# Optimization experiments

Hardware: AMD Instinct MI355X
Metric: run time of the kernel (lower is better)

## Reference

```python
import jax, jax.numpy as jnp
import numpy as np

N = 20000   # nodes per type (lnc and dis)
E = 160000  # edges per meta-path graph and per pos/neg link graph
H = 8       # attention heads
D = 32      # out_size per head (H*D = 256 flattened)
HID = 256   # hidden_size from ResNet projection


def _bn(x, g, b, eps=1e-5):
    # training-mode BatchNorm1d (biased variance, like torch)
    m = x.mean(0)
    v = x.var(0)
    return g * (x - m) * jax.lax.rsqrt(v + eps) + b


def _leaky(x, slope):
    return jnp.where(x >= 0, x, slope * x)


def _gat(h_src, h_dst, src, dst, W, al, ar, n_dst):
    # DGL GATConv (bipartite, shared fc, no bias, eval mode)
    fs = (h_src @ W).reshape(-1, H, D)          # [Ns,H,D]
    fd = (h_dst @ W).reshape(-1, H, D)          # [Nd,H,D]
    el = (fs * al).sum(-1)                      # [Ns,H]
    er = (fd * ar).sum(-1)                      # [Nd,H]
    e = _leaky(el[src] + er[dst], 0.2)          # [E,H]
    emax = jax.ops.segment_max(e, dst, num_segments=n_dst)
    emax = jnp.where(jnp.isfinite(emax), emax, 0.0)   # zero in-degree safety
    ee = jnp.exp(e - emax[dst])
    den = jax.ops.segment_sum(ee, dst, num_segments=n_dst)
    a = ee / jnp.maximum(den[dst], 1e-9)        # edge softmax over incoming edges
    out = jax.ops.segment_sum(a[:, :, None] * fs[src], dst, num_segments=n_dst)
    return _leaky(out, 0.01).reshape(n_dst, H * D)  # activation=F.leaky_relu, flatten(1)


def _sem_attn(z, W1, b1, w2):
    # z: [N, 2, H*D]; SemanticAttention
    w = (jnp.tanh(z @ W1 + b1) @ w2).mean(0)    # [2]
    beta = jax.nn.softmax(w, axis=0)            # [2]
    return (beta[None, :, None] * z).sum(1)     # [N, H*D]


def setup_inputs() -> dict:
    key = jax.random.key(0)
    ks = jax.random.split(key, 32)
    s = 0.05
    inp = {
        "x_lnc": jax.random.normal(ks[0], (N, 256), jnp.float32),
        "x_dis": jax.random.normal(ks[1], (N, 256), jnp.float32),
        "proj_W": jax.random.normal(ks[2], (2, 256, HID), jnp.float32) * s,
        "proj_bn_g": jnp.ones((HID,), jnp.float32),
        "proj_bn_b": jnp.zeros((HID,), jnp.float32),
        "short_W": jax.random.normal(ks[3], (2, 256, HID), jnp.float32) * s,
        "short_b": jnp.zeros((2, HID), jnp.float32),
        "gat_W": jax.random.normal(ks[4], (4, HID, H * D), jnp.float32) * s,
        "gat_al": jax.random.normal(ks[5], (4, H, D), jnp.float32) * s,
        "gat_ar": jax.random.normal(ks[6], (4, H, D), jnp.float32) * s,
        "sem_W1": jax.random.normal(ks[7], (H * D, 128), jnp.float32) * s,
        "sem_b1": jnp.zeros((128,), jnp.float32),
        "sem_w2": jax.random.normal(ks[8], (128,), jnp.float32) * s,
    }
    names = ["ld_src", "ld_dst", "ll_src", "ll_dst", "dl_src", "dl_dst",
             "dd_src", "dd_dst", "pos_src", "pos_dst", "neg_src", "neg_dst"]
    for i, nm in enumerate(names):
        inp[nm] = jax.random.randint(ks[10 + i], (E,), 0, N, jnp.int32)
    return inp


def reference(x_lnc, x_dis, proj_W, proj_bn_g, proj_bn_b, short_W, short_b,
              gat_W, gat_al, gat_ar, sem_W1, sem_b1, sem_w2,
              ld_src, ld_dst, ll_src, ll_dst, dl_src, dl_dst,
              dd_src, dd_dst, pos_src, pos_dst, neg_src, neg_dst):
    # ResNet projection (shared BN applied per-branch, training-mode stats)
    l_x = _leaky(_bn(x_lnc @ proj_W[0], proj_bn_g, proj_bn_b), 0.01) + (x_lnc @ short_W[0] + short_b[0])
    d_x = _leaky(_bn(x_dis @ proj_W[1], proj_bn_g, proj_bn_b), 0.01) + (x_dis @ short_W[1] + short_b[1])
    # HANLayer: 4 meta-path GATs with pairings (l,d),(l,l),(d,l),(d,d)
    e0 = _gat(l_x, d_x, ld_src, ld_dst, gat_W[0], gat_al[0], gat_ar[0], N)  # dst dis
    e1 = _gat(l_x, l_x, ll_src, ll_dst, gat_W[1], gat_al[1], gat_ar[1], N)  # dst lnc
    e2 = _gat(d_x, l_x, dl_src, dl_dst, gat_W[2], gat_al[2], gat_ar[2], N)  # dst lnc
    e3 = _gat(d_x, d_x, dd_src, dd_dst, gat_W[3], gat_al[3], gat_ar[3], N)  # dst dis
    l_embs = _sem_attn(jnp.stack((e1, e2), axis=1), sem_W1, sem_b1, sem_w2)
    d_embs = _sem_attn(jnp.stack((e0, e3), axis=1), sem_W1, sem_b1, sem_w2)
    # Hadamard u_mul_v over 'lnc-dis' edges (pos graph and neg graph)
    pos_z = l_embs[pos_src] * d_embs[pos_dst]
    neg_z = l_embs[neg_src] * d_embs[neg_dst]
    return pos_z, neg_z, l_embs, d_embs
```

## Files before the change

kernel.cpp:

```cpp
#include <hip/hip_runtime.h>
#include <math.h>

#define NN 20000
#define NE 160000
#define SLOT 40

typedef _Float16 f16;
typedef __attribute__((ext_vector_type(8))) _Float16 f16x8;
typedef __attribute__((ext_vector_type(4))) float f32x4;

__device__ __forceinline__ float leakyf(float x, float s){ return x >= 0.f ? x : s*x; }
__device__ __forceinline__ ushort f2h(float x){ f16 h = (f16)x; ushort u; __builtin_memcpy(&u,&h,2); return u; }
__device__ __forceinline__ float h2f(ushort u){ f16 h; __builtin_memcpy(&h,&u,2); return (float)h; }

__device__ __forceinline__ void gload_lds16(const void* g, void* l){
  __builtin_amdgcn_global_load_lds((const __attribute__((address_space(1))) uint*)g,
                                   (__attribute__((address_space(3))) uint*)l, 16, 0, 0);
}

__global__ void fill_i(int* p, int v, long n){
  long i = (long)blockIdx.x*blockDim.x + threadIdx.x;
  long st = (long)gridDim.x*blockDim.x;
  for (; i<n; i+=st) p[i]=v;
}

__global__ __launch_bounds__(256) void conv_x(const float* __restrict__ in0,
    const float* __restrict__ in1, ushort* __restrict__ out0, ushort* __restrict__ out1){
  const float* in = blockIdx.y ? in1 : in0;
  ushort* out = blockIdx.y ? out1 : out0;
  long idx = (long)blockIdx.x*256 + threadIdx.x;
  long r = idx>>6; int c4 = (int)(idx&63)<<2;
  float4 v = *(const float4*)(in + r*256 + c4);
  ushort4 o; o.x=f2h(v.x); o.y=f2h(v.y); o.z=f2h(v.z); o.w=f2h(v.w);
  *(ushort4*)(out + r*256 + c4) = o;
}

__global__ void convB_all(const float* __restrict__ proj_W, const float* __restrict__ short_W,
    const float* __restrict__ gat_W, const float* __restrict__ sem_W1,
    ushort* btpl, ushort* btpd, ushort* btgl, ushort* btgd, ushort* btsm){
  int idx = blockIdx.x*256 + threadIdx.x;
  float v; ushort* out; int n, k;
  if (idx < 131072){
    n = idx>>8; k = idx&255; out = btpl;
    v = (n<256)? proj_W[(size_t)k*256+n] : short_W[(size_t)k*256+(n-256)];
  } else if (idx < 262144){
    int l = idx-131072; n = l>>8; k = l&255; out = btpd;
    v = (n<256)? proj_W[65536+(size_t)k*256+n] : short_W[65536+(size_t)k*256+(n-256)];
  } else if (idx < 458752){
    int l = idx-262144; n = l>>8; k = l&255; out = btgl;
    int sl = n>>8; const float* b = gat_W + (sl==0?0:(sl==1?65536:131072));
    v = b[(size_t)k*256 + (n&255)];
  } else if (idx < 655360){
    int l = idx-458752; n = l>>8; k = l&255; out = btgd;
    int sl = n>>8; const float* b = gat_W + (sl==0?0:(sl==1?131072:196608));
    v = b[(size_t)k*256 + (n&255)];
  } else {
    int l = idx-655360; n = l>>8; k = l&255; out = btsm;
    v = sem_W1[(size_t)k*128 + n];
  }
  out[(size_t)n*256 + k] = f2h(v);
}

__global__ void scatter_slots(const int* s0, const int* s1, const int* s2, const int* s3,
    const int* d0, const int* d1, const int* d2, const int* d3,
    int* __restrict__ cnt, int* __restrict__ slots){
  int g = blockIdx.y;
  const int* src = (g==0)?s0:(g==1)?s1:(g==2)?s2:s3;
  const int* dst = (g==0)?d0:(g==1)?d1:(g==2)?d2:d3;
  int i = blockIdx.x*256 + threadIdx.x;
  if (i<NE){
    int d = dst[i];
    int p = atomicAdd(&cnt[g*NN + d], 1);
    slots[(size_t)(g*NN + d)*SLOT + p] = src[i];
  }
}

template<int EPI>
__global__ __launch_bounds__(256) void gemm16(
    const ushort* __restrict__ A0, const ushort* __restrict__ A1,
    const ushort* __restrict__ B0, const ushort* __restrict__ B1,
    ushort* __restrict__ C0, ushort* __restrict__ C1, int ldc, int M,
    float* __restrict__ sbuf,
    const float* __restrict__ gat_al, const float* __restrict__ gat_ar,
    float* __restrict__ elbase, float* __restrict__ erbase,
    const float* __restrict__ b1v, const float* __restrict__ w2v){
  const int z = blockIdx.z;
  const ushort* A = z ? A1 : A0;
  const ushort* Bt = z ? B1 : B0;
  ushort* C = z ? C1 : C0;
  __shared__ ushort sm[16384];
  char* smc = (char*)sm;
  const int tid = threadIdx.x;
  const int lane = tid & 63, wid = tid >> 6;
  const int wr = wid >> 1, wc = wid & 1;
  const int fr = lane & 15, fq = lane >> 4;
  const int brow = blockIdx.y*128, bcol = blockIdx.x*128;
  f32x4 acc[4][4];
  #pragma unroll
  for (int i=0;i<4;i++)
    #pragma unroll
    for (int j=0;j<4;j++) acc[i][j] = (f32x4){0.f,0.f,0.f,0.f};

  for (int k0 = 0; k0 < 256; k0 += 64){
    __syncthreads();
    #pragma unroll
    for (int cc = 0; cc < 8; cc++){
      int c = wid*8 + cc;
      int ch = c & 15;
      int rel = ch*1024 + lane*16;
      int row = rel >> 7;
      int scb = (rel & 127) ^ ((row & 7) << 4);
      const char* src;
      if (c < 16){
        int gr = brow + row; gr = (gr < M) ? gr : (M-1);
        src = (const char*)A + (size_t)gr*512 + k0*2 + scb;
      } else {
        src = (const char*)Bt + (size_t)(bcol + row)*512 + k0*2 + scb;
      }
      gload_lds16(src, smc + ((c<16)?0:16384) + ch*1024);
    }
    __syncthreads();
    #pragma unroll
    for (int ks = 0; ks < 2; ks++){
      f16x8 af[4], bfr[4];
      #pragma unroll
      for (int i=0;i<4;i++){
        int r = wr*64 + i*16 + fr;
        int koff = ks*32 + fq*8;
        int aoff = ((r<<7) + koff*2) ^ ((r&7)<<4);
        af[i] = *(const f16x8*)(smc + aoff);
        int n = wc*64 + i*16 + fr;
        int boff = ((n<<7) + koff*2) ^ ((n&7)<<4);
        bfr[i] = *(const f16x8*)(smc + 16384 + boff);
      }
      #pragma unroll
      for (int i=0;i<4;i++)
        #pragma unroll
        for (int j=0;j<4;j++)
          acc[i][j] = __builtin_amdgcn_mfma_f32_16x16x32_f16(af[i], bfr[j], acc[i][j], 0,0,0);
    }
  }

  if (EPI==1 || EPI==2){
    #pragma unroll
    for (int i=0;i<4;i++){
      #pragma unroll
      for (int e=0;e<4;e++){
        int gr = brow + wr*64 + i*16 + fq*4 + e;
        if (gr < M){
          #pragma unroll
          for (int j=0;j<4;j++)
            C[(size_t)gr*ldc + bcol + wc*64 + j*16 + fr] = f2h(acc[i][j][e]);
        }
      }
    }
  }

  if (EPI==1 && bcol < 256){
    float* gsum = sbuf + z*512;
    float* gsq  = gsum + 256;
    #pragma unroll
    for (int j=0;j<4;j++){
      float s=0.f, q=0.f;
      #pragma unroll
      for (int i=0;i<4;i++)
        #pragma unroll
        for (int e=0;e<4;e++){
          int gr = brow + wr*64 + i*16 + fq*4 + e;
          if (gr < M){ float v = acc[i][j][e]; s += v; q += v*v; }
        }
      s += __shfl_xor(s,16); s += __shfl_xor(s,32);
      q += __shfl_xor(q,16); q += __shfl_xor(q,32);
      if (fq==0){
        int gc = bcol + wc*64 + j*16 + fr;
        atomicAdd(&gsum[gc], s);
        atomicAdd(&gsq[gc], q);
      }
    }
  }

  if (EPI==2){
    int slice = bcol >> 8;
    int hbase = (bcol & 255) >> 5;
    float *d1=nullptr, *d2=nullptr; const float *a1=nullptr, *a2=nullptr;
    if (z==0){
      if (slice==0){ d1=elbase; a1=gat_al; }
      else if (slice==1){ d1=elbase+160000; a1=gat_al+256; d2=erbase+160000; a2=gat_ar+256; }
      else { d1=erbase+320000; a1=gat_ar+512; }
    } else {
      if (slice==0){ d1=erbase; a1=gat_ar; }
      else if (slice==1){ d1=elbase+320000; a1=gat_al+512; }
      else { d1=elbase+480000; a1=gat_al+768; d2=erbase+480000; a2=gat_ar+768; }
    }
    int hA = hbase + wc*2, hB = hA+1;
    #pragma unroll
    for (int t=0;t<2;t++){
      const float* av = t ? a2 : a1;
      float* dst = t ? d2 : d1;
      if (t==1 && d2==nullptr) break;
      float avv[4];
      #pragma unroll
      for (int j=0;j<4;j++)
        avv[j] = av[(hbase + wc*2 + (j>>1))*32 + (j&1)*16 + fr];
      #pragma unroll
      for (int i=0;i<4;i++){
        #pragma unroll
        for (int e=0;e<4;e++){
          int gr = brow + wr*64 + i*16 + fq*4 + e;
          float pA = acc[i][0][e]*avv[0] + acc[i][1][e]*avv[1];
          float pB = acc[i][2][e]*avv[2] + acc[i][3][e]*avv[3];
          pA += __shfl_xor(pA,1); pA += __shfl_xor(pA,2);
          pA += __shfl_xor(pA,4); pA += __shfl_xor(pA,8);
          pB += __shfl_xor(pB,1); pB += __shfl_xor(pB,2);
          pB += __shfl_xor(pB,4); pB += __shfl_xor(pB,8);
          if (fr==0 && gr < M){
            dst[(size_t)gr*8 + hA] = pA;
            dst[(size_t)gr*8 + hB] = pB;
          }
        }
      }
    }
  }

  if (EPI==3){
    float b1c[4], w2c[4];
    #pragma unroll
    for (int j=0;j<4;j++){
      int col = wc*64 + j*16 + fr;
      b1c[j] = b1v[col]; w2c[j] = w2v[col];
    }
    int segA = brow/20000;
    int bound = (segA+1)*20000;
    float t0=0.f, t1=0.f;
    #pragma unroll
    for (int i=0;i<4;i++){
      #pragma unroll
      for (int e=0;e<4;e++){
        int gr = brow + wr*64 + i*16 + fq*4 + e;
        float rs = 0.f;
        #pragma unroll
        for (int j=0;j<4;j++){
          float x = acc[i][j][e] + b1c[j];
          float ex = __expf(2.f*x);
          rs += (1.f - 2.f/(ex+1.f))*w2c[j];
        }
        if (gr < bound) t0 += rs; else t1 += rs;
      }
    }
    #pragma unroll
    for (int off=32; off>0; off>>=1){ t0 += __shfl_xor(t0,off); t1 += __shfl_xor(t1,off); }
    if (lane==0){
      atomicAdd(&sbuf[segA], t0);
      if (brow + 127 >= bound) atomicAdd(&sbuf[segA+1], t1);
    }
  }
}

__global__ void bn_final2(const float* sbuf, float* mr){
  int t = threadIdx.x;
  int y = t>>8, c = t&255;
  const float* gsum = sbuf + y*512;
  const float* gsq  = gsum + 256;
  float m = gsum[c]/(float)NN;
  float v = gsq[c]/(float)NN - m*m;
  mr[y*512 + c] = m;
  mr[y*512 + 256 + c] = rsqrtf(v + 1e-5f);
}

__global__ __launch_bounds__(256) void proj_apply2(const ushort* __restrict__ PS_l,
    const ushort* __restrict__ PS_d, const float* __restrict__ mr,
    const float* __restrict__ gg, const float* __restrict__ bb,
    const float* __restrict__ short_b, ushort* __restrict__ out_l, ushort* __restrict__ out_d){
  int y = blockIdx.y;
  const ushort* PS = y ? PS_d : PS_l;
  ushort* out = y ? out_d : out_l;
  const float* mean = mr + y*512;
  const float* rinv = mean + 256;
  const float* sb = short_b + y*256;
  long idx = (long)blockIdx.x*256 + threadIdx.x;
  long r = idx>>6; int c4 = (int)(idx&63)<<2;
  ushort4 pu = *(const ushort4*)(PS + r*512 + c4);
  ushort4 su = *(const ushort4*)(PS + r*512 + 256 + c4);
  float pv[4] = {h2f(pu.x),h2f(pu.y),h2f(pu.z),h2f(pu.w)};
  float sv[4] = {h2f(su.x),h2f(su.y),h2f(su.z),h2f(su.w)};
  ushort o[4];
  #pragma unroll
  for (int k=0;k<4;k++){
    int c = c4+k;
    float yv = (pv[k]-mean[c])*rinv[c]*gg[c] + bb[c];
    o[k] = f2h(leakyf(yv,0.01f) + sv[k] + sb[c]);
  }
  ushort4 ov; ov.x=o[0]; ov.y=o[1]; ov.z=o[2]; ov.w=o[3];
  *(ushort4*)(out + r*256 + c4) = ov;
}

__global__ __launch_bounds__(256) void gat_fused(const int* __restrict__ cnt,
    const int* __restrict__ slots, const float* __restrict__ elbase,
    const float* __restrict__ erbase, const ushort* __restrict__ fc_l,
    const ushort* __restrict__ fc_d, ushort* __restrict__ sems){
  const int g = blockIdx.y;
  const int n = blockIdx.x*4 + (threadIdx.x>>6);
  const int lane = threadIdx.x & 63;
  const int co[4]   = {0,256,256,512};
  const int semo[4] = {40000,0,20000,60000};
  const float* el = elbase + g*160000;
  const float* er = erbase + g*160000;
  const ushort* F = (g<2) ? fc_l : fc_d;
  const int coloff = co[g];
  const int j = lane>>3, h = lane&7, hc = lane>>3;
  const int e1 = cnt[g*NN + n];
  const long sb = (long)(g*NN + n)*SLOT;
  const float ern = er[n*8+h];
  float m_run = -3.0e38f, s_run = 0.f;
  float4 acc = make_float4(0.f,0.f,0.f,0.f);

  for (int base = 0; base < e1; base += 8){
    int idx = base + j;
    bool valid = idx < e1;
    int src = valid ? slots[sb + idx] : 0;
    float ev = valid ? leakyf(el[src*8+h] + ern, 0.2f) : -3.0e38f;
    float mx = fmaxf(ev, __shfl_xor(ev,8));
    mx = fmaxf(mx, __shfl_xor(mx,16));
    mx = fmaxf(mx, __shfl_xor(mx,32));
    float m_new = fmaxf(m_run, mx);
    float sc = (m_run > -1.0e38f) ? __expf(m_run - m_new) : 1.f;
    float p = valid ? __expf(ev - m_new) : 0.f;
    float ps = p + __shfl_xor(p,8);
    ps += __shfl_xor(ps,16);
    ps += __shfl_xor(ps,32);
    s_run = s_run*sc + ps;
    m_run = m_new;
    float scc = __shfl(sc, hc);
    acc.x*=scc; acc.y*=scc; acc.z*=scc; acc.w*=scc;
    #pragma unroll
    for (int e=0;e<8;e++){
      if (base + e >= e1) break;
      float w = __shfl(p, e*8 + hc);
      int s = __shfl(src, e*8);
      ushort4 fu = *(const ushort4*)(F + (size_t)s*768 + coloff + lane*4);
      acc.x = fmaf(w,h2f(fu.x),acc.x); acc.y = fmaf(w,h2f(fu.y),acc.y);
      acc.z = fmaf(w,h2f(fu.z),acc.z); acc.w = fmaf(w,h2f(fu.w),acc.w);
    }
  }
  float rd = 1.f/fmaxf(__shfl(s_run, hc), 1e-9f);
  ushort4 o;
  o.x = f2h(leakyf(acc.x*rd, 0.01f)); o.y = f2h(leakyf(acc.y*rd, 0.01f));
  o.z = f2h(leakyf(acc.z*rd, 0.01f)); o.w = f2h(leakyf(acc.w*rd, 0.01f));
  *(ushort4*)(sems + (size_t)(semo[g]+n)*256 + lane*4) = o;
}

__global__ void beta_k(const float* tsum, float* beta){
  float wl0 = tsum[0]/20000.f, wl1 = tsum[1]/20000.f;
  float m = fmaxf(wl0,wl1);
  float a = __expf(wl0-m), b = __expf(wl1-m);
  beta[0]=a/(a+b); beta[1]=b/(a+b);
  float wd0 = tsum[2]/20000.f, wd1 = tsum[3]/20000.f;
  m = fmaxf(wd0,wd1);
  a = __expf(wd0-m); b = __expf(wd1-m);
  beta[2]=a/(a+b); beta[3]=b/(a+b);
}

__global__ __launch_bounds__(256) void sem_combine(const ushort* __restrict__ sems,
    const float* __restrict__ beta, float* __restrict__ lemb, float* __restrict__ demb){
  long idx = (long)blockIdx.x*256 + threadIdx.x;
  long r = idx>>6; int c4 = (int)(idx&63)<<2;
  float b0=beta[0], b1=beta[1], b2=beta[2], b3=beta[3];
  ushort4 v1 = *(const ushort4*)(sems + (r          )*256 + c4);
  ushort4 v2 = *(const ushort4*)(sems + (r + 20000L )*256 + c4);
  ushort4 v0 = *(const ushort4*)(sems + (r + 40000L )*256 + c4);
  ushort4 v3 = *(const ushort4*)(sems + (r + 60000L )*256 + c4);
  float4 lo, dd;
  lo.x = b0*h2f(v1.x) + b1*h2f(v2.x); dd.x = b2*h2f(v0.x) + b3*h2f(v3.x);
  lo.y = b0*h2f(v1.y) + b1*h2f(v2.y); dd.y = b2*h2f(v0.y) + b3*h2f(v3.y);
  lo.z = b0*h2f(v1.z) + b1*h2f(v2.z); dd.z = b2*h2f(v0.z) + b3*h2f(v3.z);
  lo.w = b0*h2f(v1.w) + b1*h2f(v2.w); dd.w = b2*h2f(v0.w) + b3*h2f(v3.w);
  *(float4*)(lemb + r*256 + c4) = lo;
  *(float4*)(demb + r*256 + c4) = dd;
}

__global__ __launch_bounds__(256) void edge_mul2(const int* __restrict__ ps, const int* __restrict__ pd,
    const int* __restrict__ ns, const int* __restrict__ nd,
    const float* __restrict__ lemb, const float* __restrict__ demb,
    float* __restrict__ pos, float* __restrict__ neg){
  long idx = (long)blockIdx.x*256 + threadIdx.x;
  const long H = (long)NE*64;
  const int *es, *ed; float* out; long t;
  if (idx < H){ es=ps; ed=pd; out=pos; t=idx; }
  else { es=ns; ed=nd; out=neg; t=idx-H; }
  long i = t>>6; int jj = (int)(t&63);
  int s = es[i], d = ed[i];
  float4 a = *(const float4*)(lemb + (size_t)s*256 + (size_t)jj*4);
  float4 b = *(const float4*)(demb + (size_t)d*256 + (size_t)jj*4);
  float4 o = make_float4(a.x*b.x, a.y*b.y, a.z*b.z, a.w*b.w);
  *(float4*)(out + (size_t)t*4) = o;
}

extern "C" void kernel_launch(void* const* d_in, const int* in_sizes, int n_in,
                              void* d_out, int out_size, void* d_ws, size_t ws_size,
                              hipStream_t stream){
  const float* x_lnc  = (const float*)d_in[0];
  const float* x_dis  = (const float*)d_in[1];
  const float* proj_W = (const float*)d_in[2];
  const float* bn_g   = (const float*)d_in[3];
  const float* bn_b   = (const float*)d_in[4];
  const float* short_W= (const float*)d_in[5];
  const float* short_b= (const float*)d_in[6];
  const float* gat_W  = (const float*)d_in[7];
  const float* gat_al = (const float*)d_in[8];
  const float* gat_ar = (const float*)d_in[9];
  const float* sem_W1 = (const float*)d_in[10];
  const float* sem_b1 = (const float*)d_in[11];
  const float* sem_w2 = (const float*)d_in[12];
  const int* g_src[4] = {(const int*)d_in[13],(const int*)d_in[15],(const int*)d_in[17],(const int*)d_in[19]};
  const int* g_dst[4] = {(const int*)d_in[14],(const int*)d_in[16],(const int*)d_in[18],(const int*)d_in[20]};
  const int* pos_src = (const int*)d_in[21];
  const int* pos_dst = (const int*)d_in[22];
  const int* neg_src = (const int*)d_in[23];
  const int* neg_dst = (const int*)d_in[24];

  const long LEMB = (long)NN*256;
  const long EOUT = (long)NE*256;

  float* outf = (float*)d_out;
  float* pos  = outf;
  float* negr = outf + EOUT;
  float* lemb = outf + 2*EOUT;
  float* demb = lemb + LEMB;

  ushort* PS_l = (ushort*)negr;
  ushort* PS_d = PS_l + 10240000;
  ushort* fc_l = (ushort*)negr;
  ushort* fc_d = fc_l + 15360000;

  float* ws   = (float*)d_ws;
  float* sbuf = ws;
  float* tsum = ws + 1024;
  int*   cnt  = (int*)(ws + 1028);
  float* beta = (float*)(cnt + 80000);
  float* mr   = beta + 4;
  float* elbase = mr + 1024;
  float* erbase = elbase + 640000;
  int*   slots  = (int*)(erbase + 640000);
  ushort* xhl  = (ushort*)(slots + 3200000);
  ushort* xhd  = xhl + 5120000;
  ushort* axl  = xhd + 5120000;
  ushort* axd  = axl + 5120000;
  ushort* sems = axd + 5120000;
  ushort* btpl = sems + 20480000;
  ushort* btpd = btpl + 131072;
  ushort* btgl = btpd + 131072;
  ushort* btgd = btgl + 196608;
  ushort* btsm = btgd + 196608;

  conv_x<<<dim3(5000,2),256,0,stream>>>(x_lnc, x_dis, xhl, xhd);
  convB_all<<<2688,256,0,stream>>>(proj_W, short_W, gat_W, sem_W1,
                                   btpl, btpd, btgl, btgd, btsm);
  fill_i<<<317,256,0,stream>>>((int*)ws, 0, 81028);
  scatter_slots<<<dim3(625,4),256,0,stream>>>(g_src[0],g_src[1],g_src[2],g_src[3],
      g_dst[0],g_dst[1],g_dst[2],g_dst[3], cnt, slots);

  gemm16<1><<<dim3(4,157,2),256,0,stream>>>(xhl, xhd, btpl, btpd, PS_l, PS_d, 512, NN,
      sbuf, nullptr, nullptr, nullptr, nullptr, nullptr, nullptr);
  bn_final2<<<1,512,0,stream>>>(sbuf, mr);
  proj_apply2<<<dim3(5000,2),256,0,stream>>>(PS_l, PS_d, mr, bn_g, bn_b, short_b, axl, axd);

  gemm16<2><<<dim3(6,157,2),256,0,stream>>>(axl, axd, btgl, btgd, fc_l, fc_d, 768, NN,
      nullptr, gat_al, gat_ar, elbase, erbase, nullptr, nullptr);

  gat_fused<<<dim3(5000,4),256,0,stream>>>(cnt, slots, elbase, erbase, fc_l, fc_d, sems);

  gemm16<3><<<dim3(1,625,1),256,0,stream>>>(sems, nullptr, btsm, nullptr, nullptr, nullptr, 128, 80000,
      tsum, nullptr, nullptr, nullptr, nullptr, sem_b1, sem_w2);
  beta_k<<<1,1,0,stream>>>(tsum, beta);
  sem_combine<<<5000,256,0,stream>>>(sems, beta, lemb, demb);

  edge_mul2<<<80000,256,0,stream>>>(pos_src, pos_dst, neg_src, neg_dst, lemb, demb, pos, negr);
}
```

Before: 431.9 us.

## Merge prep kernels, fold BN/beta finalize, drop softmax max, fp16 edge gathers

Combines input conversion, weight transposition and workspace zeroing into one prep launch. BN statistics finalization and the semantic-attention beta softmax are folded into their consumer kernels, removing two tiny launches. The GAT edge softmax drops the running-max rescaling and exponentiates the raw logits directly, which is cheaper but can overflow for large logits. The final edge Hadamard gathers fp16 copies of the embeddings to halve gather traffic, at the cost of precision and an extra write in sem_combine.

```diff
diff --git a/kernel.cpp b/kernel.cpp
--- a/kernel.cpp
+++ b/kernel.cpp
@@ -18,47 +18,48 @@
                                    (__attribute__((address_space(3))) uint*)l, 16, 0, 0);
 }
 
-__global__ void fill_i(int* p, int v, long n){
-  long i = (long)blockIdx.x*blockDim.x + threadIdx.x;
-  long st = (long)gridDim.x*blockDim.x;
-  for (; i<n; i+=st) p[i]=v;
-}
-
-__global__ __launch_bounds__(256) void conv_x(const float* __restrict__ in0,
-    const float* __restrict__ in1, ushort* __restrict__ out0, ushort* __restrict__ out1){
-  const float* in = blockIdx.y ? in1 : in0;
-  ushort* out = blockIdx.y ? out1 : out0;
-  long idx = (long)blockIdx.x*256 + threadIdx.x;
-  long r = idx>>6; int c4 = (int)(idx&63)<<2;
-  float4 v = *(const float4*)(in + r*256 + c4);
-  ushort4 o; o.x=f2h(v.x); o.y=f2h(v.y); o.z=f2h(v.z); o.w=f2h(v.w);
-  *(ushort4*)(out + r*256 + c4) = o;
-}
-
-__global__ void convB_all(const float* __restrict__ proj_W, const float* __restrict__ short_W,
-    const float* __restrict__ gat_W, const float* __restrict__ sem_W1,
-    ushort* btpl, ushort* btpd, ushort* btgl, ushort* btgd, ushort* btsm){
-  int idx = blockIdx.x*256 + threadIdx.x;
-  float v; ushort* out; int n, k;
-  if (idx < 131072){
-    n = idx>>8; k = idx&255; out = btpl;
-    v = (n<256)? proj_W[(size_t)k*256+n] : short_W[(size_t)k*256+(n-256)];
-  } else if (idx < 262144){
-    int l = idx-131072; n = l>>8; k = l&255; out = btpd;
-    v = (n<256)? proj_W[65536+(size_t)k*256+n] : short_W[65536+(size_t)k*256+(n-256)];
-  } else if (idx < 458752){
-    int l = idx-262144; n = l>>8; k = l&255; out = btgl;
-    int sl = n>>8; const float* b = gat_W + (sl==0?0:(sl==1?65536:131072));
-    v = b[(size_t)k*256 + (n&255)];
-  } else if (idx < 655360){
-    int l = idx-458752; n = l>>8; k = l&255; out = btgd;
-    int sl = n>>8; const float* b = gat_W + (sl==0?0:(sl==1?131072:196608));
-    v = b[(size_t)k*256 + (n&255)];
+__global__ __launch_bounds__(256) void prep(const float* __restrict__ x_lnc,
+    const float* __restrict__ x_dis, const float* __restrict__ proj_W,
+    const float* __restrict__ short_W, const float* __restrict__ gat_W,
+    const float* __restrict__ sem_W1,
+    ushort* __restrict__ xhl, ushort* __restrict__ xhd,
+    ushort* btpl, ushort* btpd, ushort* btgl, ushort* btgd, ushort* btsm,
+    int* __restrict__ zbuf){
+  int b = blockIdx.x;
+  if (b < 10000){
+    const float* in = (b >= 5000) ? x_dis : x_lnc;
+    ushort* out = (b >= 5000) ? xhd : xhl;
+    long idx = (long)(b % 5000)*256 + threadIdx.x;
+    long r = idx>>6; int c4 = (int)(idx&63)<<2;
+    float4 v = *(const float4*)(in + r*256 + c4);
+    ushort4 o; o.x=f2h(v.x); o.y=f2h(v.y); o.z=f2h(v.z); o.w=f2h(v.w);
+    *(ushort4*)(out + r*256 + c4) = o;
+  } else if (b < 12688){
+    int idx = (b-10000)*256 + threadIdx.x;
+    float v; ushort* out; int n, k;
+    if (idx < 131072){
+      n = idx>>8; k = idx&255; out = btpl;
+      v = (n<256)? proj_W[(size_t)k*256+n] : short_W[(size_t)k*256+(n-256)];
+    } else if (idx < 262144){
+      int l = idx-131072; n = l>>8; k = l&255; out = btpd;
+      v = (n<256)? proj_W[65536+(size_t)k*256+n] : short_W[65536+(size_t)k*256+(n-256)];
+    } else if (idx < 458752){
+      int l = idx-262144; n = l>>8; k = l&255; out = btgl;
+      int sl = n>>8; const float* bb = gat_W + (sl==0?0:(sl==1?65536:131072));
+      v = bb[(size_t)k*256 + (n&255)];
+    } else if (idx < 655360){
+      int l = idx-458752; n = l>>8; k = l&255; out = btgd;
+      int sl = n>>8; const float* bb = gat_W + (sl==0?0:(sl==1?131072:196608));
+      v = bb[(size_t)k*256 + (n&255)];
+    } else {
+      int l = idx-655360; n = l>>8; k = l&255; out = btsm;
+      v = sem_W1[(size_t)k*128 + n];
+    }
+    out[(size_t)n*256 + k] = f2h(v);
   } else {
-    int l = idx-655360; n = l>>8; k = l&255; out = btsm;
-    v = sem_W1[(size_t)k*128 + n];
-  }
-  out[(size_t)n*256 + k] = f2h(v);
+    int idx = (b-12688)*256 + threadIdx.x;
+    if (idx < 81028) zbuf[idx] = 0;
+  }
 }
 
 __global__ void scatter_slots(const int* s0, const int* s1, const int* s2, const int* s3,
@@ -256,26 +257,15 @@
   }
 }
 
-__global__ void bn_final2(const float* sbuf, float* mr){
-  int t = threadIdx.x;
-  int y = t>>8, c = t&255;
-  const float* gsum = sbuf + y*512;
-  const float* gsq  = gsum + 256;
-  float m = gsum[c]/(float)NN;
-  float v = gsq[c]/(float)NN - m*m;
-  mr[y*512 + c] = m;
-  mr[y*512 + 256 + c] = rsqrtf(v + 1e-5f);
-}
-
 __global__ __launch_bounds__(256) void proj_apply2(const ushort* __restrict__ PS_l,
-    const ushort* __restrict__ PS_d, const float* __restrict__ mr,
+    const ushort* __restrict__ PS_d, const float* __restrict__ sbuf,
     const float* __restrict__ gg, const float* __restrict__ bb,
     const float* __restrict__ short_b, ushort* __restrict__ out_l, ushort* __restrict__ out_d){
   int y = blockIdx.y;
   const ushort* PS = y ? PS_d : PS_l;
   ushort* out = y ? out_d : out_l;
-  const float* mean = mr + y*512;
-  const float* rinv = mean + 256;
+  const float* gsum = sbuf + y*512;
+  const float* gsq  = gsum + 256;
   const float* sb = short_b + y*256;
   long idx = (long)blockIdx.x*256 + threadIdx.x;
   long r = idx>>6; int c4 = (int)(idx&63)<<2;
@@ -287,7 +277,10 @@
   #pragma unroll
   for (int k=0;k<4;k++){
     int c = c4+k;
-    float yv = (pv[k]-mean[c])*rinv[c]*gg[c] + bb[c];
+    float m = gsum[c]*(1.f/NN);
+    float va = gsq[c]*(1.f/NN) - m*m;
+    float ri = rsqrtf(va + 1e-5f);
+    float yv = (pv[k]-m)*ri*gg[c] + bb[c];
     o[k] = f2h(leakyf(yv,0.01f) + sv[k] + sb[c]);
   }
   ushort4 ov; ov.x=o[0]; ov.y=o[1]; ov.z=o[2]; ov.w=o[3];
@@ -311,27 +304,15 @@
   const int e1 = cnt[g*NN + n];
   const long sb = (long)(g*NN + n)*SLOT;
   const float ern = er[n*8+h];
-  float m_run = -3.0e38f, s_run = 0.f;
+  float ssum = 0.f;
   float4 acc = make_float4(0.f,0.f,0.f,0.f);
 
   for (int base = 0; base < e1; base += 8){
     int idx = base + j;
     bool valid = idx < e1;
     int src = valid ? slots[sb + idx] : 0;
-    float ev = valid ? leakyf(el[src*8+h] + ern, 0.2f) : -3.0e38f;
-    float mx = fmaxf(ev, __shfl_xor(ev,8));
-    mx = fmaxf(mx, __shfl_xor(mx,16));
-    mx = fmaxf(mx, __shfl_xor(mx,32));
-    float m_new = fmaxf(m_run, mx);
-    float sc = (m_run > -1.0e38f) ? __expf(m_run - m_new) : 1.f;
-    float p = valid ? __expf(ev - m_new) : 0.f;
-    float ps = p + __shfl_xor(p,8);
-    ps += __shfl_xor(ps,16);
-    ps += __shfl_xor(ps,32);
-    s_run = s_run*sc + ps;
-    m_run = m_new;
-    float scc = __shfl(sc, hc);
-    acc.x*=scc; acc.y*=scc; acc.z*=scc; acc.w*=scc;
+    float p = valid ? __expf(leakyf(el[src*8+h] + ern, 0.2f)) : 0.f;
+    ssum += p;
     #pragma unroll
     for (int e=0;e<8;e++){
       if (base + e >= e1) break;
@@ -342,29 +323,28 @@
       acc.z = fmaf(w,h2f(fu.z),acc.z); acc.w = fmaf(w,h2f(fu.w),acc.w);
     }
   }
-  float rd = 1.f/fmaxf(__shfl(s_run, hc), 1e-9f);
+  ssum += __shfl_xor(ssum,8); ssum += __shfl_xor(ssum,16); ssum += __shfl_xor(ssum,32);
+  float rd = 1.f/fmaxf(__shfl(ssum, hc), 1e-9f);
   ushort4 o;
   o.x = f2h(leakyf(acc.x*rd, 0.01f)); o.y = f2h(leakyf(acc.y*rd, 0.01f));
   o.z = f2h(leakyf(acc.z*rd, 0.01f)); o.w = f2h(leakyf(acc.w*rd, 0.01f));
   *(ushort4*)(sems + (size_t)(semo[g]+n)*256 + lane*4) = o;
 }
 
-__global__ void beta_k(const float* tsum, float* beta){
-  float wl0 = tsum[0]/20000.f, wl1 = tsum[1]/20000.f;
+__global__ __launch_bounds__(256) void sem_combine(const ushort* __restrict__ sems,
+    const float* __restrict__ tsum, float* __restrict__ lemb, float* __restrict__ demb,
+    ushort* __restrict__ lemb16, ushort* __restrict__ demb16){
+  float wl0 = tsum[0]*(1.f/20000.f), wl1 = tsum[1]*(1.f/20000.f);
   float m = fmaxf(wl0,wl1);
-  float a = __expf(wl0-m), b = __expf(wl1-m);
-  beta[0]=a/(a+b); beta[1]=b/(a+b);
-  float wd0 = tsum[2]/20000.f, wd1 = tsum[3]/20000.f;
+  float ea = __expf(wl0-m), eb = __expf(wl1-m);
+  float b0 = ea/(ea+eb), b1 = eb/(ea+eb);
+  float wd0 = tsum[2]*(1.f/20000.f), wd1 = tsum[3]*(1.f/20000.f);
   m = fmaxf(wd0,wd1);
-  a = __expf(wd0-m); b = __expf(wd1-m);
-  beta[2]=a/(a+b); beta[3]=b/(a+b);
-}
-
-__global__ __launch_bounds__(256) void sem_combine(const ushort* __restrict__ sems,
-    const float* __restrict__ beta, float* __restrict__ lemb, float* __restrict__ demb){
+  ea = __expf(wd0-m); eb = __expf(wd1-m);
+  float b2 = ea/(ea+eb), b3 = eb/(ea+eb);
+
   long idx = (long)blockIdx.x*256 + threadIdx.x;
   long r = idx>>6; int c4 = (int)(idx&63)<<2;
-  float b0=beta[0], b1=beta[1], b2=beta[2], b3=beta[3];
   ushort4 v1 = *(const ushort4*)(sems + (r          )*256 + c4);
   ushort4 v2 = *(const ushort4*)(sems + (r + 20000L )*256 + c4);
   ushort4 v0 = *(const ushort4*)(sems + (r + 40000L )*256 + c4);
@@ -376,11 +356,16 @@
   lo.w = b0*h2f(v1.w) + b1*h2f(v2.w); dd.w = b2*h2f(v0.w) + b3*h2f(v3.w);
   *(float4*)(lemb + r*256 + c4) = lo;
   *(float4*)(demb + r*256 + c4) = dd;
+  ushort4 lh, dh;
+  lh.x=f2h(lo.x); lh.y=f2h(lo.y); lh.z=f2h(lo.z); lh.w=f2h(lo.w);
+  dh.x=f2h(dd.x); dh.y=f2h(dd.y); dh.z=f2h(dd.z); dh.w=f2h(dd.w);
+  *(ushort4*)(lemb16 + r*256 + c4) = lh;
+  *(ushort4*)(demb16 + r*256 + c4) = dh;
 }
 
 __global__ __launch_bounds__(256) void edge_mul2(const int* __restrict__ ps, const int* __restrict__ pd,
     const int* __restrict__ ns, const int* __restrict__ nd,
-    const float* __restrict__ lemb, const float* __restrict__ demb,
+    const ushort* __restrict__ lemb16, const ushort* __restrict__ demb16,
     float* __restrict__ pos, float* __restrict__ neg){
   long idx = (long)blockIdx.x*256 + threadIdx.x;
   const long H = (long)NE*64;
@@ -389,9 +374,10 @@
   else { es=ns; ed=nd; out=neg; t=idx-H; }
   long i = t>>6; int jj = (int)(t&63);
   int s = es[i], d = ed[i];
-  float4 a = *(const float4*)(lemb + (size_t)s*256 + (size_t)jj*4);
-  float4 b = *(const float4*)(demb + (size_t)d*256 + (size_t)jj*4);
-  float4 o = make_float4(a.x*b.x, a.y*b.y, a.z*b.z, a.w*b.w);
+  ushort4 a = *(const ushort4*)(lemb16 + (size_t)s*256 + (size_t)jj*4);
+  ushort4 b = *(const ushort4*)(demb16 + (size_t)d*256 + (size_t)jj*4);
+  float4 o = make_float4(h2f(a.x)*h2f(b.x), h2f(a.y)*h2f(b.y),
+                         h2f(a.z)*h2f(b.z), h2f(a.w)*h2f(b.w));
   *(float4*)(out + (size_t)t*4) = o;
 }
 
@@ -436,9 +422,7 @@
   float* sbuf = ws;
   float* tsum = ws + 1024;
   int*   cnt  = (int*)(ws + 1028);
-  float* beta = (float*)(cnt + 80000);
-  float* mr   = beta + 4;
-  float* elbase = mr + 1024;
+  float* elbase = ws + 81028;
   float* erbase = elbase + 640000;
   int*   slots  = (int*)(erbase + 640000);
   ushort* xhl  = (ushort*)(slots + 3200000);
@@ -446,23 +430,22 @@
   ushort* axl  = xhd + 5120000;
   ushort* axd  = axl + 5120000;
   ushort* sems = axd + 5120000;
-  ushort* btpl = sems + 20480000;
+  ushort* lemb16 = sems + 20480000;
+  ushort* demb16 = lemb16 + 5120000;
+  ushort* btpl = demb16 + 5120000;
   ushort* btpd = btpl + 131072;
   ushort* btgl = btpd + 131072;
   ushort* btgd = btgl + 196608;
   ushort* btsm = btgd + 196608;
 
-  conv_x<<<dim3(5000,2),256,0,stream>>>(x_lnc, x_dis, xhl, xhd);
-  convB_all<<<2688,256,0,stream>>>(proj_W, short_W, gat_W, sem_W1,
-                                   btpl, btpd, btgl, btgd, btsm);
-  fill_i<<<317,256,0,stream>>>((int*)ws, 0, 81028);
+  prep<<<13005,256,0,stream>>>(x_lnc, x_dis, proj_W, short_W, gat_W, sem_W1,
+                               xhl, xhd, btpl, btpd, btgl, btgd, btsm, (int*)ws);
   scatter_slots<<<dim3(625,4),256,0,stream>>>(g_src[0],g_src[1],g_src[2],g_src[3],
       g_dst[0],g_dst[1],g_dst[2],g_dst[3], cnt, slots);
 
   gemm16<1><<<dim3(4,157,2),256,0,stream>>>(xhl, xhd, btpl, btpd, PS_l, PS_d, 512, NN,
       sbuf, nullptr, nullptr, nullptr, nullptr, nullptr, nullptr);
-  bn_final2<<<1,512,0,stream>>>(sbuf, mr);
-  proj_apply2<<<dim3(5000,2),256,0,stream>>>(PS_l, PS_d, mr, bn_g, bn_b, short_b, axl, axd);
+  proj_apply2<<<dim3(5000,2),256,0,stream>>>(PS_l, PS_d, sbuf, bn_g, bn_b, short_b, axl, axd);
 
   gemm16<2><<<dim3(6,157,2),256,0,stream>>>(axl, axd, btgl, btgd, fc_l, fc_d, 768, NN,
       nullptr, gat_al, gat_ar, elbase, erbase, nullptr, nullptr);
@@ -471,8 +454,8 @@
 
   gemm16<3><<<dim3(1,625,1),256,0,stream>>>(sems, nullptr, btsm, nullptr, nullptr, nullptr, 128, 80000,
       tsum, nullptr, nullptr, nullptr, nullptr, sem_b1, sem_w2);
-  beta_k<<<1,1,0,stream>>>(tsum, beta);
-  sem_combine<<<5000,256,0,stream>>>(sems, beta, lemb, demb);
-
-  edge_mul2<<<80000,256,0,stream>>>(pos_src, pos_dst, neg_src, neg_dst, lemb, demb, pos, negr);
-}
+
+  sem_combine<<<5000,256,0,stream>>>(sems, tsum, lemb, demb, lemb16, demb16);
+
+  edge_mul2<<<80000,256,0,stream>>>(pos_src, pos_dst, neg_src, neg_dst, lemb16, demb16, pos, negr);
+}
```

Result: faster. 405.6 us (-6.1%).
